# Kernel optimization log

Measured on AMD Instinct MI355X. Metric: run time of the kernel, lower is better.

The kernel has to match this reference:

```python
import jax, jax.numpy as jnp
import numpy as np

EPS1 = 1e-8
EPS2 = 1e-5
H_BW = 1.0  # bandwidth h
MSE_W = 1.0
CTX_W = 1.0
PERC_W = 0.02


def _contextual_similarity(out_feat, tgt_feat):
    """Batched contextual similarity (Mechrez et al. 2018).

    out_feat, tgt_feat: [B, C, Hf, Wf]. Returns scalar (mean over batch).
    Matches the torch loop-over-samples / loop-over-target-vectors math,
    fully vectorized as one batched pairwise-cosine + softmax + max.
    """
    B, C = out_feat.shape[0], out_feat.shape[1]
    # X, Y: [B, N, C] with N = Hf*Wf spatial positions
    X = out_feat.reshape(B, C, -1).transpose(0, 2, 1)
    Y = tgt_feat.reshape(B, C, -1).transpose(0, 2, 1)
    X = X - X.mean(axis=1, keepdims=True)  # center per channel over positions
    Y = Y - Y.mean(axis=1, keepdims=True)
    xn = jnp.linalg.norm(X, axis=2)  # [B, N]
    yn = jnp.linalg.norm(Y, axis=2)  # [B, N]
    # cosine distance d[b, x, y] = 1 - <X_x, Y_y> / (|X_x||Y_y| + eps1)
    S = jnp.einsum('bxc,byc->bxy', X, Y)
    d = 1.0 - S / (xn[:, :, None] * yn[:, None, :] + EPS1)
    # normalize by min over target vectors y (torch: dxy.min(dim=0) with dxy [Ny, Nx])
    d_ = d / (d.min(axis=2, keepdims=True) + EPS2)
    w = jnp.exp((1.0 - d_) / H_BW)
    c = w / w.sum(axis=2, keepdims=True)  # softmax over y per x
    # torch: cxy.max(dim=1)[0].mean() -> max over x for each y, mean over y
    CS = c.max(axis=1).mean(axis=1)  # [B]
    return CS.mean()


def _mse(a, b):
    return jnp.mean((a - b) ** 2)


def setup_inputs() -> dict:
    key = jax.random.key(0)
    k1, k2, k3, k4 = jax.random.split(key, 4)
    outputs = jax.random.normal(k1, (4, 3, 256, 256), dtype=jnp.float32)
    targets = jax.random.normal(k2, (4, 3, 256, 256), dtype=jnp.float32)
    output_features = jax.random.normal(k3, (4, 256, 64, 64), dtype=jnp.float32)
    target_features = jax.random.normal(k4, (4, 256, 64, 64), dtype=jnp.float32)
    return {"outputs": outputs, "targets": targets,
            "output_features": output_features, "target_features": target_features}


def reference(outputs, targets, output_features, target_features):
    loss = MSE_W * _mse(outputs, targets)
    loss = loss - CTX_W * jnp.log(_contextual_similarity(output_features, target_features))
    loss = loss + PERC_W * _mse(output_features, target_features)
    return loss
```

## Files before the change

kernel.cpp:

```cpp
#include <hip/hip_runtime.h>
#include <hip/hip_bf16.h>
#include <cstdint>

#define EPS2f 1e-5f
#define LOG2E 1.44269504f

typedef __bf16 bf16x8 __attribute__((ext_vector_type(8)));
typedef float floatx4 __attribute__((ext_vector_type(4)));
typedef float floatx2 __attribute__((ext_vector_type(2)));

static constexpr int Bn = 4, Cn = 256, Nn = 4096;

static constexpr size_t MSE1P = 0;
static constexpr size_t MSE2P = 256;
static constexpr size_t CSP   = 1536;
static constexpr size_t MEANX = 2560;
static constexpr size_t MEANY = 3584;
static constexpr size_t IXN   = 4608;
static constexpr size_t IYN   = 20992;
static constexpr size_t DMIN  = 37376;
static constexpr size_t RSUM  = 53760;
static constexpr size_t XCO   = 70144;
static constexpr size_t YCO   = 70144 + 2097152;
static constexpr size_t SOFF  = 70144 + 2 * 2097152;

__device__ __forceinline__ unsigned short f2bf(float f) {
    unsigned u = __float_as_uint(f);
    u += 0x7fffu + ((u >> 16) & 1u);
    return (unsigned short)(u >> 16);
}

__global__ __launch_bounds__(256) void prep1(const float4* __restrict__ outs,
                                             const float4* __restrict__ tgts,
                                             const float4* __restrict__ of4,
                                             const float4* __restrict__ tf4,
                                             float* __restrict__ ws) {
    const int bid = blockIdx.x, t = threadIdx.x;
    __shared__ float red[12];
    if (bid < 1024) {
        const int c = bid & 255, b = bid >> 8;
        const float4* po = of4 + ((size_t)b * Cn + c) * (Nn / 4);
        const float4* pt = tf4 + ((size_t)b * Cn + c) * (Nn / 4);
        float so = 0.f, st = 0.f, sq = 0.f;
        for (int i = t; i < 1024; i += 256) {
            float4 o = po[i], q = pt[i];
            so += o.x + o.y + o.z + o.w;
            st += q.x + q.y + q.z + q.w;
            float dx = o.x - q.x, dy = o.y - q.y, dz = o.z - q.z, dw = o.w - q.w;
            sq += dx * dx + dy * dy + dz * dz + dw * dw;
        }
        for (int m = 1; m < 64; m <<= 1) {
            so += __shfl_xor(so, m); st += __shfl_xor(st, m); sq += __shfl_xor(sq, m);
        }
        if ((t & 63) == 0) { int w = t >> 6; red[w * 3] = so; red[w * 3 + 1] = st; red[w * 3 + 2] = sq; }
        __syncthreads();
        if (t == 0) {
            so = red[0] + red[3] + red[6] + red[9];
            st = red[1] + red[4] + red[7] + red[10];
            sq = red[2] + red[5] + red[8] + red[11];
            ws[MEANX + b * Cn + c] = so * (1.f / 4096.f);
            ws[MEANY + b * Cn + c] = st * (1.f / 4096.f);
            ws[MSE2P + bid] = sq;
        }
    } else if (bid < 1216) {
        const int base = bid - 1024;
        float sq = 0.f;
        for (int i = base * 256 + t; i < 196608; i += 192 * 256) {
            float4 a = outs[i], b4 = tgts[i];
            float dx = a.x - b4.x, dy = a.y - b4.y, dz = a.z - b4.z, dw = a.w - b4.w;
            sq += dx * dx + dy * dy + dz * dz + dw * dw;
        }
        for (int m = 1; m < 64; m <<= 1) sq += __shfl_xor(sq, m);
        if ((t & 63) == 0) red[t >> 6] = sq;
        __syncthreads();
        if (t == 0) ws[MSE1P + base] = red[0] + red[1] + red[2] + red[3];
    } else {
        const int i = (bid - 1216) * 256 + t;
        ws[DMIN + i] = (i < 16384) ? __builtin_inff() : 0.f;
    }
}

__global__ __launch_bounds__(256) void center_fused(const float* __restrict__ ofeat,
                                                    const float* __restrict__ tfeat,
                                                    float* __restrict__ ws) {
    const int b = blockIdx.y, nb = blockIdx.x, z = blockIdx.z;
    const float* feat = z ? tfeat : ofeat;
    const float* mean = ws + (z ? MEANY : MEANX);
    unsigned short* outb = (unsigned short*)(ws + (z ? YCO : XCO));
    float* inv = ws + (z ? IYN : IXN);
    __shared__ float mean_s[256];
    __shared__ float sq_s[256];
    const int t = threadIdx.x;
    mean_s[t] = mean[b * Cn + t];
    __syncthreads();
    const int pos = t & 63, cg = t >> 6;
    const int n = nb * 64 + pos;
    const float* fb = feat + (size_t)b * Cn * Nn;
    unsigned short* ob = outb + ((size_t)b * Nn + n) * Cn;
    float ss = 0.f;
    for (int c0 = cg * 64; c0 < cg * 64 + 64; c0 += 8) {
        unsigned short tmp[8];
        #pragma unroll
        for (int u = 0; u < 8; ++u) {
            float v = fb[(size_t)(c0 + u) * Nn + n] - mean_s[c0 + u];
            ss += v * v;
            tmp[u] = f2bf(v);
        }
        uint4 pk;
        pk.x = (unsigned)tmp[0] | ((unsigned)tmp[1] << 16);
        pk.y = (unsigned)tmp[2] | ((unsigned)tmp[3] << 16);
        pk.z = (unsigned)tmp[4] | ((unsigned)tmp[5] << 16);
        pk.w = (unsigned)tmp[6] | ((unsigned)tmp[7] << 16);
        *(uint4*)(ob + c0) = pk;
    }
    sq_s[t] = ss;
    __syncthreads();
    if (t < 64) {
        float s = sq_s[t] + sq_s[t + 64] + sq_s[t + 128] + sq_s[t + 192];
        inv[(size_t)b * Nn + nb * 64 + t] = 1.f / sqrtf(s);
    }
}

__global__ __launch_bounds__(256) void gemm_store(const unsigned short* __restrict__ Xc,
                                                  const unsigned short* __restrict__ Yc,
                                                  const float* __restrict__ ixn,
                                                  const float* __restrict__ iyn,
                                                  float* __restrict__ dmin,
                                                  unsigned char* __restrict__ S) {
    __shared__ __align__(16) unsigned short smem[16384];
    __shared__ float ixn_s[128], iyn_s[128];

    const int t = threadIdx.x;
    const int lin = blockIdx.x;
    const int xcd = lin & 7, idx = lin >> 3;
    const int b = xcd >> 1;
    const int by = (xcd & 1) * 16 + (idx & 15);
    const int bx = idx >> 4;
    const size_t nb = (size_t)b * Nn;

    if (t < 128) ixn_s[t] = ixn[nb + bx * 128 + t];
    else iyn_s[t - 128] = iyn[nb + by * 128 + (t - 128)];

    const int wid = t >> 6, lane = t & 63;
    const int wm = wid >> 1, wn = wid & 1;
    const int lr = lane & 15, lq = lane >> 4;
    const int srow = t >> 2, sq = t & 3;

    const unsigned short* Ag = Xc + (nb + bx * 128) * Cn;
    const unsigned short* Bg = Yc + (nb + by * 128) * Cn;
    const unsigned short* Ga0 = Ag + (size_t)srow * Cn + sq * 8;
    const unsigned short* Ga1 = Ag + (size_t)(srow + 64) * Cn + sq * 8;
    const unsigned short* Gb0 = Bg + (size_t)srow * Cn + sq * 8;
    const unsigned short* Gb1 = Bg + (size_t)(srow + 64) * Cn + sq * 8;
    const int wA0 = (sq * 128 + srow) * 8;
    const int wA1 = (sq * 128 + srow + 64) * 8;

    floatx4 acc[4][4];
    #pragma unroll
    for (int i = 0; i < 4; i++)
        #pragma unroll
        for (int j = 0; j < 4; j++) acc[i][j] = (floatx4){0.f, 0.f, 0.f, 0.f};

    {
        uint4 a0 = *(const uint4*)Ga0, a1 = *(const uint4*)Ga1;
        uint4 b0 = *(const uint4*)Gb0, b1 = *(const uint4*)Gb1;
        *(uint4*)(smem + wA0) = a0;
        *(uint4*)(smem + wA1) = a1;
        *(uint4*)(smem + 4096 + wA0) = b0;
        *(uint4*)(smem + 4096 + wA1) = b1;
    }
    __syncthreads();

    #pragma unroll
    for (int ks = 0; ks < 8; ks++) {
        const int cur = (ks & 1) * 8192, nxt = 8192 - cur;
        uint4 a0, a1, b0, b1;
        if (ks < 7) {
            a0 = *(const uint4*)(Ga0 + (ks + 1) * 32);
            a1 = *(const uint4*)(Ga1 + (ks + 1) * 32);
            b0 = *(const uint4*)(Gb0 + (ks + 1) * 32);
            b1 = *(const uint4*)(Gb1 + (ks + 1) * 32);
        }
        bf16x8 af[4], bv[4];
        #pragma unroll
        for (int i = 0; i < 4; i++)
            af[i] = *(const bf16x8*)(smem + cur + (lq * 128 + wm * 64 + i * 16 + lr) * 8);
        #pragma unroll
        for (int j = 0; j < 4; j++)
            bv[j] = *(const bf16x8*)(smem + cur + 4096 + (lq * 128 + wn * 64 + j * 16 + lr) * 8);
        #pragma unroll
        for (int i = 0; i < 4; i++)
            #pragma unroll
            for (int j = 0; j < 4; j++)
                acc[i][j] = __builtin_amdgcn_mfma_f32_16x16x32_bf16(af[i], bv[j], acc[i][j], 0, 0, 0);
        if (ks < 7) {
            *(uint4*)(smem + nxt + wA0) = a0;
            *(uint4*)(smem + nxt + wA1) = a1;
            *(uint4*)(smem + nxt + 4096 + wA0) = b0;
            *(uint4*)(smem + nxt + 4096 + wA1) = b1;
            __syncthreads();
        }
    }

    float ix[16];
    #pragma unroll
    for (int i = 0; i < 4; i++)
        #pragma unroll
        for (int r = 0; r < 4; r++) ix[i * 4 + r] = ixn_s[wm * 64 + i * 16 + lq * 4 + r];
    float rmin[16];
    #pragma unroll
    for (int k = 0; k < 16; k++) rmin[k] = __builtin_inff();
    #pragma unroll
    for (int i = 0; i < 4; i++)
        #pragma unroll
        for (int j = 0; j < 4; j++) {
            const float iy = iyn_s[wn * 64 + j * 16 + lr];
            #pragma unroll
            for (int r = 0; r < 4; r++)
                rmin[i * 4 + r] = fminf(rmin[i * 4 + r], 1.f - acc[i][j][r] * ix[i * 4 + r] * iy);
        }
    #pragma unroll
    for (int m = 1; m < 16; m <<= 1)
        #pragma unroll
        for (int k = 0; k < 16; k++) rmin[k] = fminf(rmin[k], __shfl_xor(rmin[k], m));
    if (lr == 0) {
        #pragma unroll
        for (int i = 0; i < 4; i++)
            #pragma unroll
            for (int r = 0; r < 4; r++)
                atomicMin((int*)&dmin[nb + bx * 128 + wm * 64 + i * 16 + lq * 4 + r],
                          __float_as_int(rmin[i * 4 + r]));
    }

    unsigned char* Tb = (unsigned char*)smem;
    #pragma unroll
    for (int i = 0; i < 4; i++) {
        const int xlocal = wm * 64 + i * 16 + lq * 4;
        #pragma unroll
        for (int j = 0; j < 4; j++) {
            const int ylocal = wn * 64 + j * 16 + lr;
            const float iy = iyn_s[ylocal];
            float c0 = acc[i][j][0] * ix[i * 4 + 0] * iy;
            float c1 = acc[i][j][1] * ix[i * 4 + 1] * iy;
            float c2 = acc[i][j][2] * ix[i * 4 + 2] * iy;
            float c3 = acc[i][j][3] * ix[i * 4 + 3] * iy;
            int pk = __builtin_amdgcn_cvt_pk_fp8_f32(c0, c1, 0, false);
            pk = __builtin_amdgcn_cvt_pk_fp8_f32(c2, c3, pk, true);
            *(int*)(Tb + ylocal * 128 + (xlocal ^ ((ylocal & 7) << 4))) = pk;
        }
    }
    __syncthreads();

    #pragma unroll
    for (int p = 0; p < 4; p++) {
        const int row = p * 32 + wid * 8 + (lane >> 3);
        const int ch = lane & 7;
        uint4 v = *(const uint4*)(Tb + row * 128 + ((ch * 16) ^ ((row & 7) << 4)));
        *(uint4*)(S + (nb + by * 128 + row) * (size_t)Nn + bx * 128 + ch * 16) = v;
    }
}

__global__ __launch_bounds__(256) void b1_rsum(const unsigned char* __restrict__ S,
                                               const float* __restrict__ dmin,
                                               float* __restrict__ rsum) {
    __shared__ float red[32 * 65];
    const int t = threadIdx.x;
    const int x0 = blockIdx.x * 64, ys = blockIdx.y, b = blockIdx.z;
    const int chunk = t & 7, yg = t >> 3;
    const int xbase = x0 + chunk * 8;
    const size_t gb = (size_t)b * Nn;

    float ivl[8], avl[8];
    #pragma unroll
    for (int u = 0; u < 8; u++) {
        float iv = 1.f / (dmin[gb + xbase + u] + EPS2f);
        ivl[u] = iv * LOG2E;
        avl[u] = (1.f - iv) * LOG2E;
    }
    float s[8];
    #pragma unroll
    for (int u = 0; u < 8; u++) s[u] = 0.f;

    for (int k = 0; k < 16; k++) {
        const int y = ys * 512 + yg + 32 * k;
        uint2 w = *(const uint2*)(S + (gb + y) * Nn + xbase);
        floatx2 v0 = __builtin_amdgcn_cvt_pk_f32_fp8(w.x, false);
        floatx2 v1 = __builtin_amdgcn_cvt_pk_f32_fp8(w.x, true);
        floatx2 v2 = __builtin_amdgcn_cvt_pk_f32_fp8(w.y, false);
        floatx2 v3 = __builtin_amdgcn_cvt_pk_f32_fp8(w.y, true);
        float c[8] = {v0[0], v0[1], v1[0], v1[1], v2[0], v2[1], v3[0], v3[1]};
        #pragma unroll
        for (int u = 0; u < 8; u++)
            s[u] += exp2f(fmaf(c[u], ivl[u], avl[u]));
    }
    #pragma unroll
    for (int u = 0; u < 8; u++) red[yg * 65 + chunk * 8 + u] = s[u];
    __syncthreads();
    if (t < 64) {
        float rs = 0.f;
        #pragma unroll 8
        for (int g = 0; g < 32; g++) rs += red[g * 65 + t];
        atomicAdd(&rsum[gb + x0 + t], rs);
    }
}

__global__ __launch_bounds__(256) void b2_cmax(const unsigned char* __restrict__ S,
                                               const float* __restrict__ dmin,
                                               const float* __restrict__ rsum,
                                               float* __restrict__ csp) {
    __shared__ float ps[512 * 20];
    __shared__ float red2[16];
    const int t = threadIdx.x, b = blockIdx.y;
    const size_t gb = (size_t)b * Nn;
    for (int i = t; i < Nn; i += 256) {
        float iv = 1.f / (dmin[gb + i] + EPS2f);
        float ivl = iv * LOG2E;
        float ggl = (1.f - iv) * LOG2E - __log2f(rsum[gb + i]);
        int c = i >> 3, e = i & 7;
        ps[c * 20 + e * 2] = ivl;
        ps[c * 20 + e * 2 + 1] = ggl;
    }
    __syncthreads();

    const int lanegrp = t & 15, yloc = t >> 4;
    const int y = blockIdx.x * 16 + yloc;
    const unsigned char* Sy = S + (gb + y) * Nn;

    float cm = -1e30f;
    for (int k = 0; k < 32; k++) {
        const int chunk = lanegrp + 16 * k;
        uint2 w = *(const uint2*)(Sy + chunk * 8);
        floatx2 v0 = __builtin_amdgcn_cvt_pk_f32_fp8(w.x, false);
        floatx2 v1 = __builtin_amdgcn_cvt_pk_f32_fp8(w.x, true);
        floatx2 v2 = __builtin_amdgcn_cvt_pk_f32_fp8(w.y, false);
        floatx2 v3 = __builtin_amdgcn_cvt_pk_f32_fp8(w.y, true);
        float c[8] = {v0[0], v0[1], v1[0], v1[1], v2[0], v2[1], v3[0], v3[1]};
        const float* pp = &ps[chunk * 20];
        float4 p01 = *(const float4*)(pp);
        float4 p23 = *(const float4*)(pp + 4);
        float4 p45 = *(const float4*)(pp + 8);
        float4 p67 = *(const float4*)(pp + 12);
        float iv[8] = {p01.x, p01.z, p23.x, p23.z, p45.x, p45.z, p67.x, p67.z};
        float gg[8] = {p01.y, p01.w, p23.y, p23.w, p45.y, p45.w, p67.y, p67.w};
        #pragma unroll
        for (int u = 0; u < 8; u++)
            cm = fmaxf(cm, fmaf(c[u], iv[u], gg[u]));
    }
    #pragma unroll
    for (int m = 1; m < 16; m <<= 1) cm = fmaxf(cm, __shfl_xor(cm, m));
    if (lanegrp == 0) red2[yloc] = exp2f(cm);
    __syncthreads();
    if (t == 0) {
        float s2 = 0.f;
        #pragma unroll
        for (int i = 0; i < 16; i++) s2 += red2[i];
        csp[b * 256 + blockIdx.x] = s2;
    }
}

__global__ __launch_bounds__(256) void finalize_kernel(const float* __restrict__ ws,
                                                       float* __restrict__ out) {
    const int t = threadIdx.x;
    float s1 = 0.f, s2 = 0.f, s3 = 0.f;
    if (t < 192) s1 = ws[MSE1P + t];
    for (int i = t; i < 1024; i += 256) { s2 += ws[MSE2P + i]; s3 += ws[CSP + i]; }
    for (int m = 1; m < 64; m <<= 1) {
        s1 += __shfl_xor(s1, m); s2 += __shfl_xor(s2, m); s3 += __shfl_xor(s3, m);
    }
    __shared__ float red[12];
    if ((t & 63) == 0) { int w = t >> 6; red[w * 3] = s1; red[w * 3 + 1] = s2; red[w * 3 + 2] = s3; }
    __syncthreads();
    if (t == 0) {
        s1 = red[0] + red[3] + red[6] + red[9];
        s2 = red[1] + red[4] + red[7] + red[10];
        s3 = red[2] + red[5] + red[8] + red[11];
        float cs = s3 * (1.f / 16384.f);
        out[0] = s1 * (1.f / 786432.f) - logf(cs) + 0.02f * s2 * (1.f / 4194304.f);
    }
}

extern "C" void kernel_launch(void* const* d_in, const int* in_sizes, int n_in,
                              void* d_out, int out_size, void* d_ws, size_t ws_size,
                              hipStream_t stream) {
    const float* outputs = (const float*)d_in[0];
    const float* targets = (const float*)d_in[1];
    const float* ofeat   = (const float*)d_in[2];
    const float* tfeat   = (const float*)d_in[3];
    float* ws  = (float*)d_ws;
    float* out = (float*)d_out;

    unsigned short* Xc = (unsigned short*)(ws + XCO);
    unsigned short* Yc = (unsigned short*)(ws + YCO);
    unsigned char* S = (unsigned char*)(ws + SOFF);

    prep1<<<1344, 256, 0, stream>>>((const float4*)outputs, (const float4*)targets,
                                    (const float4*)ofeat, (const float4*)tfeat, ws);
    center_fused<<<dim3(Nn / 64, Bn, 2), 256, 0, stream>>>(ofeat, tfeat, ws);
    gemm_store<<<4096, 256, 0, stream>>>(Xc, Yc, ws + IXN, ws + IYN, ws + DMIN, S);
    b1_rsum<<<dim3(64, 8, Bn), 256, 0, stream>>>(S, ws + DMIN, ws + RSUM);
    b2_cmax<<<dim3(Nn / 16, Bn), 256, 0, stream>>>(S, ws + DMIN, ws + RSUM, ws + CSP);
    finalize_kernel<<<1, 256, 0, stream>>>(ws, out);
}
```

Measured before the change: 257.8 us.

## Fuse finalize into b2_cmax via last-block ticket and simplify GEMM grid mapping

Removes the separate single-block finalize launch by having each b2_cmax block take an atomic ticket after writing its partial; the last block performs the final reduction and writes the loss. The ticket counter is reset in prep1. Separately, the GEMM grid is changed from a 1D XCD-aware swizzled index to a plain 3D grid, dropping the L2 locality mapping across XCDs. This saves one launch and its gap, but risks worse L2 reuse in the GEMM.

```diff
diff --git a/kernel.cpp b/kernel.cpp
--- a/kernel.cpp
+++ b/kernel.cpp
@@ -13,6 +13,7 @@
 
 static constexpr size_t MSE1P = 0;
 static constexpr size_t MSE2P = 256;
+static constexpr size_t DONE  = 1280;
 static constexpr size_t CSP   = 1536;
 static constexpr size_t MEANX = 2560;
 static constexpr size_t MEANY = 3584;
@@ -73,7 +74,10 @@
         for (int m = 1; m < 64; m <<= 1) sq += __shfl_xor(sq, m);
         if ((t & 63) == 0) red[t >> 6] = sq;
         __syncthreads();
-        if (t == 0) ws[MSE1P + base] = red[0] + red[1] + red[2] + red[3];
+        if (t == 0) {
+            ws[MSE1P + base] = red[0] + red[1] + red[2] + red[3];
+            if (base == 0) *(unsigned int*)(ws + DONE) = 0u;
+        }
     } else {
         const int i = (bid - 1216) * 256 + t;
         ws[DMIN + i] = (i < 16384) ? __builtin_inff() : 0.f;
@@ -131,11 +135,7 @@
     __shared__ float ixn_s[128], iyn_s[128];
 
     const int t = threadIdx.x;
-    const int lin = blockIdx.x;
-    const int xcd = lin & 7, idx = lin >> 3;
-    const int b = xcd >> 1;
-    const int by = (xcd & 1) * 16 + (idx & 15);
-    const int bx = idx >> 4;
+    const int bx = blockIdx.x, by = blockIdx.y, b = blockIdx.z;
     const size_t nb = (size_t)b * Nn;
 
     if (t < 128) ixn_s[t] = ixn[nb + bx * 128 + t];
@@ -305,11 +305,14 @@
 }
 
 __global__ __launch_bounds__(256) void b2_cmax(const unsigned char* __restrict__ S,
-                                               const float* __restrict__ dmin,
-                                               const float* __restrict__ rsum,
-                                               float* __restrict__ csp) {
+                                               float* __restrict__ ws,
+                                               float* __restrict__ out) {
+    const float* dmin = ws + DMIN;
+    const float* rsum = ws + RSUM;
+    float* csp = ws + CSP;
     __shared__ float ps[512 * 20];
     __shared__ float red2[16];
+    __shared__ unsigned int ticket_s;
     const int t = threadIdx.x, b = blockIdx.y;
     const size_t gb = (size_t)b * Nn;
     for (int i = t; i < Nn; i += 256) {
@@ -355,27 +358,28 @@
         #pragma unroll
         for (int i = 0; i < 16; i++) s2 += red2[i];
         csp[b * 256 + blockIdx.x] = s2;
-    }
-}
-
-__global__ __launch_bounds__(256) void finalize_kernel(const float* __restrict__ ws,
-                                                       float* __restrict__ out) {
-    const int t = threadIdx.x;
-    float s1 = 0.f, s2 = 0.f, s3 = 0.f;
-    if (t < 192) s1 = ws[MSE1P + t];
-    for (int i = t; i < 1024; i += 256) { s2 += ws[MSE2P + i]; s3 += ws[CSP + i]; }
-    for (int m = 1; m < 64; m <<= 1) {
-        s1 += __shfl_xor(s1, m); s2 += __shfl_xor(s2, m); s3 += __shfl_xor(s3, m);
-    }
-    __shared__ float red[12];
-    if ((t & 63) == 0) { int w = t >> 6; red[w * 3] = s1; red[w * 3 + 1] = s2; red[w * 3 + 2] = s3; }
-    __syncthreads();
-    if (t == 0) {
-        s1 = red[0] + red[3] + red[6] + red[9];
-        s2 = red[1] + red[4] + red[7] + red[10];
-        s3 = red[2] + red[5] + red[8] + red[11];
-        float cs = s3 * (1.f / 16384.f);
-        out[0] = s1 * (1.f / 786432.f) - logf(cs) + 0.02f * s2 * (1.f / 4194304.f);
+        __threadfence();
+        ticket_s = atomicAdd((unsigned int*)(ws + DONE), 1u);
+    }
+    __syncthreads();
+    if (ticket_s == 1023u) {
+        __threadfence();
+        float s1 = 0.f, s2 = 0.f, s3 = 0.f;
+        if (t < 192) s1 = ws[MSE1P + t];
+        for (int i = t; i < 1024; i += 256) { s2 += ws[MSE2P + i]; s3 += ws[CSP + i]; }
+        for (int m = 1; m < 64; m <<= 1) {
+            s1 += __shfl_xor(s1, m); s2 += __shfl_xor(s2, m); s3 += __shfl_xor(s3, m);
+        }
+        __shared__ float red[12];
+        if ((t & 63) == 0) { int w = t >> 6; red[w * 3] = s1; red[w * 3 + 1] = s2; red[w * 3 + 2] = s3; }
+        __syncthreads();
+        if (t == 0) {
+            s1 = red[0] + red[3] + red[6] + red[9];
+            s2 = red[1] + red[4] + red[7] + red[10];
+            s3 = red[2] + red[5] + red[8] + red[11];
+            float cs = s3 * (1.f / 16384.f);
+            out[0] = s1 * (1.f / 786432.f) - logf(cs) + 0.02f * s2 * (1.f / 4194304.f);
+        }
     }
 }
 
@@ -396,8 +400,7 @@
     prep1<<<1344, 256, 0, stream>>>((const float4*)outputs, (const float4*)targets,
                                     (const float4*)ofeat, (const float4*)tfeat, ws);
     center_fused<<<dim3(Nn / 64, Bn, 2), 256, 0, stream>>>(ofeat, tfeat, ws);
-    gemm_store<<<4096, 256, 0, stream>>>(Xc, Yc, ws + IXN, ws + IYN, ws + DMIN, S);
+    gemm_store<<<dim3(32, 32, 4), 256, 0, stream>>>(Xc, Yc, ws + IXN, ws + IYN, ws + DMIN, S);
     b1_rsum<<<dim3(64, 8, Bn), 256, 0, stream>>>(S, ws + DMIN, ws + RSUM);
-    b2_cmax<<<dim3(Nn / 16, Bn), 256, 0, stream>>>(S, ws + DMIN, ws + RSUM, ws + CSP);
-    finalize_kernel<<<1, 256, 0, stream>>>(ws, out);
-}
+    b2_cmax<<<dim3(Nn / 16, Bn), 256, 0, stream>>>(S, ws, out);
+}
```

Result: no change. 256.5 us (-0.5%).
